# Optimization experiments

Hardware: AMD Instinct MI355X
Metric: run time of the kernel (lower is better)

Reference implementation:

```python
import jax, jax.numpy as jnp
import numpy as np

D_MODEL = 1024
D_K = 1024
B, T = 4, 2048


def setup_inputs() -> dict:
    key = jax.random.key(0)
    kx, kq, kk, kv = jax.random.split(key, 4)
    s = 1.0 / np.sqrt(D_MODEL)
    return {
        "x": jax.random.normal(kx, (B, T, D_MODEL), dtype=jnp.float32),
        "W_q": jax.random.normal(kq, (D_MODEL, D_K), dtype=jnp.float32) * s,
        "W_k": jax.random.normal(kk, (D_MODEL, D_K), dtype=jnp.float32) * s,
        "W_v": jax.random.normal(kv, (D_MODEL, D_K), dtype=jnp.float32) * s,
    }


def reference(x, W_q, W_k, W_v):
    # x: (B, T, C); W_*: (C, d_k). Linear(no bias) == x @ W
    q = jnp.einsum('btc,ck->btk', x, W_q)
    k = jnp.einsum('btc,ck->btk', x, W_k)
    v = jnp.einsum('btc,ck->btk', x, W_v)
    d_k = W_q.shape[1]
    scores = jnp.einsum('bqk,bsk->bqs', q, k) / jnp.sqrt(jnp.asarray(d_k, x.dtype))
    T_ = x.shape[1]
    causal = jnp.tril(jnp.ones((T_, T_), dtype=bool))
    scores = jnp.where(causal, scores, jnp.asarray(-jnp.inf, scores.dtype))
    weights = jax.nn.softmax(scores, axis=-1)
    return jnp.einsum('bqs,bsk->bqk', weights, v)
```

## Files before the change

kernel.cpp:

```cpp
#include <hip/hip_runtime.h>
#include <hip/hip_bf16.h>
#include <stdint.h>

typedef __bf16 bf16x8 __attribute__((ext_vector_type(8)));
typedef float  f32x4  __attribute__((ext_vector_type(4)));
typedef unsigned int u32x4 __attribute__((ext_vector_type(4)));

__device__ __forceinline__ unsigned short f2bf(float x) {
    union { float f; unsigned u; } v; v.f = x;
    unsigned r = v.u + 0x7fffu + ((v.u >> 16) & 1u);
    return (unsigned short)(r >> 16);
}

__device__ __forceinline__ float bf2f(unsigned short b) {
    union { unsigned u; float f; } v; v.u = ((unsigned)b) << 16; return v.f;
}

__device__ __forceinline__ void async16(const void* g, void* l) {
    __builtin_amdgcn_global_load_lds(
        (const __attribute__((address_space(1))) void*)g,
        (__attribute__((address_space(3))) void*)l,
        16, 0, 0);
}

template <typename OutT, bool CAUSAL_SKIP, bool KLIMIT, bool VFOLD>
__global__ __launch_bounds__(256, 3) void gemm_bt(
    const unsigned short* __restrict__ A,
    const unsigned short* __restrict__ Bt,
    OutT* __restrict__ C,
    unsigned short* __restrict__ VtOut,
    int M, int N, int K, int lda, int ldb, int ldc,
    int ldvt, int nsplit,
    long long sA, long long sB, long long sC, long long sVt, float scale)
{
    const int bn = blockIdx.x, bz = blockIdx.z;
    const int bm = KLIMIT ? (gridDim.y - 1 - blockIdx.y) : blockIdx.y;
    if (CAUSAL_SKIP && bn > bm) return;

    A  += (long long)bz * sA;
    Bt += (long long)bz * sB;
    C  += (long long)bz * sC;

    const int m0 = bm * 128, n0 = bn * 128;
    const int Keff = KLIMIT ? min(K, (bm + 1) * 128) : K;

    __shared__ __align__(16) unsigned short LDS[2 * 2 * 128 * 32];

    const int tid  = threadIdx.x;
    const int w    = tid >> 6, l = tid & 63;
    const int wr   = w >> 1,  wc = w & 1;
    const int lrow = l & 15,  quad = l >> 4;

    f32x4 acc[4][4] = {};

    const int rA0  = 32 * w + (l >> 2);
    const int cOff = (((l & 3) ^ ((l >> 3) & 3))) * 8;
    const unsigned short* aG0 = A  + (long long)(m0 + rA0)      * lda + cOff;
    const unsigned short* aG1 = A  + (long long)(m0 + rA0 + 16) * lda + cOff;
    const unsigned short* bG0 = Bt + (long long)(n0 + rA0)      * ldb + cOff;
    const unsigned short* bG1 = Bt + (long long)(n0 + rA0 + 16) * ldb + cOff;
    unsigned short* aL = &LDS[(2 * w) * 512 + l * 8];
    unsigned short* bL = aL + 4096;

    const int sl = (lrow >> 1) & 3;

    async16(aG0, aL);
    async16(aG1, aL + 512);
    async16(bG0, bL);
    async16(bG1, bL + 512);

    for (int k0 = 0; k0 < Keff; k0 += 32) {
        const int cur = ((k0 >> 5) & 1) * 8192;
        __syncthreads();

        if (k0 + 32 < Keff) {
            const int nxt = cur ^ 8192;
            async16(aG0 + k0 + 32, aL + nxt);
            async16(aG1 + k0 + 32, aL + nxt + 512);
            async16(bG0 + k0 + 32, bL + nxt);
            async16(bG1 + k0 + 32, bL + nxt + 512);
        }

        const unsigned short* As = &LDS[cur];
        const unsigned short* Bs = &LDS[cur + 4096];
        bf16x8 af[4], bfr[4];
#pragma unroll
        for (int i = 0; i < 4; i++) {
            af[i]  = *(const bf16x8*)&As[(wr * 64 + i * 16 + lrow) * 32 + (quad ^ sl) * 8];
            bfr[i] = *(const bf16x8*)&Bs[(wc * 64 + i * 16 + lrow) * 32 + (quad ^ sl) * 8];
        }
#pragma unroll
        for (int i = 0; i < 4; i++)
#pragma unroll
            for (int j = 0; j < 4; j++)
                acc[i][j] = __builtin_amdgcn_mfma_f32_16x16x32_bf16(af[i], bfr[j], acc[i][j], 0, 0, 0);
    }

    if constexpr (VFOLD) {
        if (n0 >= nsplit) {
            unsigned short* Vp = VtOut + (long long)bz * sVt;
#pragma unroll
            for (int i = 0; i < 4; i++) {
                const int t = m0 + wr * 64 + i * 16 + quad * 4;
#pragma unroll
                for (int j = 0; j < 4; j++) {
                    const int d = (n0 - nsplit) + wc * 64 + j * 16 + lrow;
                    union { unsigned short u[4]; uint2 p; } o;
#pragma unroll
                    for (int r = 0; r < 4; r++) o.u[r] = f2bf(acc[i][j][r] * scale);
                    *(uint2*)(Vp + (long long)d * ldvt + t) = o.p;
                }
            }
            return;
        }
    }

    __syncthreads();

    char* eb = (char*)LDS + w * 2288;
    const int erow = l >> 2, ep = l & 3;

    if constexpr (sizeof(OutT) == 2) {
#pragma unroll
        for (int i = 0; i < 4; i++) {
#pragma unroll
            for (int j = 0; j < 4; j++)
#pragma unroll
                for (int r = 0; r < 4; r++)
                    *(unsigned short*)(eb + (quad * 4 + r) * 144 + (j * 16 + lrow) * 2) =
                        f2bf(acc[i][j][r] * scale);
            const long long gm = m0 + wr * 64 + i * 16 + erow;
#pragma unroll
            for (int c = 0; c < 2; c++) {
                u32x4 d = *(u32x4*)(eb + erow * 144 + ep * 32 + c * 16);
                *(u32x4*)((unsigned short*)C + gm * ldc + (n0 + wc * 64 + ep * 16 + c * 8)) = d;
            }
        }
    } else {
#pragma unroll
        for (int i = 0; i < 4; i++) {
            const long long gm = m0 + wr * 64 + i * 16 + erow;
#pragma unroll
            for (int jc = 0; jc < 2; jc++) {
#pragma unroll
                for (int jj = 0; jj < 2; jj++)
#pragma unroll
                    for (int r = 0; r < 4; r++)
                        *(float*)(eb + (quad * 4 + r) * 144 + (jj * 16 + lrow) * 4) =
                            acc[i][2 * jc + jj][r] * scale;
#pragma unroll
                for (int c = 0; c < 2; c++) {
                    f32x4 d = *(f32x4*)(eb + erow * 144 + ep * 32 + c * 16);
                    *(f32x4*)((float*)C + gm * ldc + (n0 + wc * 64 + jc * 32 + ep * 8 + c * 4)) = d;
                }
            }
        }
    }
}

__global__ __launch_bounds__(256) void cast_f32_bf16(
    const float4* __restrict__ in, unsigned short* __restrict__ out, int n4)
{
    int i = blockIdx.x * 256 + threadIdx.x;
    if (i >= n4) return;
    float4 v = in[i];
    union { unsigned short u[4]; uint2 p; } o;
    o.u[0] = f2bf(v.x); o.u[1] = f2bf(v.y); o.u[2] = f2bf(v.z); o.u[3] = f2bf(v.w);
    *(uint2*)(out + (long long)i * 4) = o.p;
}

__global__ __launch_bounds__(256) void transpose_cast_w3(
    const float* __restrict__ W0, const float* __restrict__ W1,
    const float* __restrict__ W2, unsigned short* __restrict__ out, int n)
{
    const float* in = (blockIdx.z == 0) ? W0 : (blockIdx.z == 1) ? W1 : W2;
    out += (long long)blockIdx.z * n * n;
    __shared__ float tile[32][33];
    const int tx = threadIdx.x, ty = threadIdx.y;
    const int c0 = blockIdx.x * 32, r0 = blockIdx.y * 32;
#pragma unroll
    for (int i = 0; i < 4; i++)
        tile[ty + i * 8][tx] = in[(long long)(r0 + ty + i * 8) * n + c0 + tx];
    __syncthreads();
#pragma unroll
    for (int i = 0; i < 4; i++)
        out[(long long)(c0 + ty + i * 8) * n + r0 + tx] = f2bf(tile[tx][ty + i * 8]);
}

__global__ __launch_bounds__(256) void causal_softmax_bf16(
    const unsigned short* __restrict__ S, unsigned short* __restrict__ P, int T)
{
    const int row = blockIdx.x;
    const int t   = row & (T - 1);
    const int L   = t + 1;
    const unsigned short* s = S + (long long)row * T;
    unsigned short* p = P + (long long)row * T;
    const int tid  = threadIdx.x;
    const int base = tid * 8;

    uint4 raw = *(const uint4*)(s + base);
    unsigned rr[4] = {raw.x, raw.y, raw.z, raw.w};
    float v[8];
#pragma unroll
    for (int k = 0; k < 4; k++) {
        union { unsigned u; float f; } a, b;
        a.u = (rr[k] & 0xFFFFu) << 16;
        b.u = rr[k] & 0xFFFF0000u;
        v[2 * k] = a.f; v[2 * k + 1] = b.f;
    }
    float mx = -3.0e38f;
#pragma unroll
    for (int k = 0; k < 8; k++) {
        if (base + k >= L) v[k] = -3.0e38f;
        mx = fmaxf(mx, v[k]);
    }
#pragma unroll
    for (int off = 32; off; off >>= 1) mx = fmaxf(mx, __shfl_xor(mx, off));
    __shared__ float red[4], red2[4];
    const int wid = tid >> 6, lid = tid & 63;
    if (lid == 0) red[wid] = mx;
    __syncthreads();
    mx = fmaxf(fmaxf(red[0], red[1]), fmaxf(red[2], red[3]));

    float sum = 0.f;
#pragma unroll
    for (int k = 0; k < 8; k++) { v[k] = __expf(v[k] - mx); sum += v[k]; }
#pragma unroll
    for (int off = 32; off; off >>= 1) sum += __shfl_xor(sum, off);
    if (lid == 0) red2[wid] = sum;
    __syncthreads();
    sum = red2[0] + red2[1] + red2[2] + red2[3];
    const float inv = 1.0f / sum;

    union { unsigned short u[8]; uint4 q; } o;
#pragma unroll
    for (int k = 0; k < 8; k++) o.u[k] = f2bf(v[k] * inv);
    *(uint4*)(p + base) = o.q;
}

extern "C" void kernel_launch(void* const* d_in, const int* in_sizes, int n_in,
                              void* d_out, int out_size, void* d_ws, size_t ws_size,
                              hipStream_t stream)
{
    const int B = 4, T = 2048, C = 1024, D = 1024;
    const float* x  = (const float*)d_in[0];
    const float* Wq = (const float*)d_in[1];
    const float* Wk = (const float*)d_in[2];
    const float* Wv = (const float*)d_in[3];
    float* out = (float*)d_out;
    char* ws = (char*)d_ws;

    const size_t MB = 1ull << 20;
    unsigned short* Xbf   = (unsigned short*)(ws + 0);
    unsigned short* WqkvT = (unsigned short*)(ws + 16 * MB);
    unsigned short* QK    = (unsigned short*)(ws + 22 * MB);
    unsigned short* Vt    = (unsigned short*)(ws + 54 * MB);
    unsigned short* Sbf   = (unsigned short*)(ws + 70 * MB);
    unsigned short* P     = (unsigned short*)(ws + 0);

    const long long sX  = (long long)T * C;
    const long long sQK = (long long)T * 2 * D;
    const long long sVt = (long long)D * T;
    const long long sS  = (long long)T * T;
    const long long sO  = (long long)T * D;

    {
        int n4 = B * T * C / 4;
        cast_f32_bf16<<<dim3((n4 + 255) / 256), dim3(256), 0, stream>>>(
            (const float4*)x, Xbf, n4);
    }
    {
        dim3 g(32, 32, 3), b(32, 8);
        transpose_cast_w3<<<g, b, 0, stream>>>(Wq, Wk, Wv, WqkvT, 1024);
    }
    {
        dim3 g(3072 / 128, 2048 / 128, 4), b(256);
        gemm_bt<unsigned short, false, false, true><<<g, b, 0, stream>>>(
            Xbf, WqkvT, QK, Vt, 2048, 3072, 1024, 1024, 1024, 2048,
             T,  2048, sX, 0, sQK, sVt, 1.0f);
    }
    {
        dim3 g(2048 / 128, 2048 / 128, 4), b(256);
        gemm_bt<unsigned short, true, false, false><<<g, b, 0, stream>>>(
            QK, QK + D, Sbf, nullptr, 2048, 2048, 1024, 2 * D, 2 * D, 2048,
            0, 0, sQK, sQK, sS, 0, 0.03125f);
    }
    {
        causal_softmax_bf16<<<dim3(B * T), dim3(256), 0, stream>>>(Sbf, P, T);
    }
    {
        dim3 g(1024 / 128, 2048 / 128, 4), b(256);
        gemm_bt<float, false, true, false><<<g, b, 0, stream>>>(
            P, Vt, out, nullptr, 2048, 1024, 2048, 2048, 2048, 1024,
            0, 0, sS, sVt, sO, 0, 1.0f);
    }
    (void)in_sizes; (void)n_in; (void)out_size; (void)ws_size;
}
```

Measured before the change: 252.3 us.

## Add 256x256-tile QKV projection GEMM with 8-wave ping-pong LDS pipeline

Replaces the 128x128-tile QKV projection GEMM with a dedicated kernel that uses 256x256 output tiles, 512 threads, a double-buffered 128KB LDS ring with swizzled async global-to-LDS loads, and an interleaved load/MFMA schedule with barriers and priority hints. It also remaps block indices for L2 locality. The goal is to raise arithmetic intensity and overlap memory traffic with MFMA work in the largest GEMM. Separately, the launch bound occupancy hint on the generic gemm_bt is raised from 3 to 4, which may constrain registers. Large LDS use limits occupancy to one block per CU, and the grid is only 384 blocks.

```diff
diff --git a/kernel.cpp b/kernel.cpp
--- a/kernel.cpp
+++ b/kernel.cpp
@@ -23,8 +23,165 @@
         16, 0, 0);
 }
 
+__global__ __launch_bounds__(512, 2) void gemm256_qkv(
+    const unsigned short* __restrict__ A,
+    const unsigned short* __restrict__ Bt,
+    unsigned short* __restrict__ C,
+    unsigned short* __restrict__ VtOut,
+    int K, int lda, int ldb, int ldc, int ldvt, int nsplit,
+    long long sA, long long sC, long long sVt)
+{
+    __shared__ __align__(16) char LDS[131072];
+    const int o = blockIdx.y * gridDim.x + blockIdx.x;
+    const int xc = o & 7, rr_ = o >> 3;
+    const int bn = (xc & 3) * 3 + (rr_ % 3);
+    const int bm = (xc >> 2) * 4 + (rr_ / 3);
+    const int bz = blockIdx.z;
+    const int m0 = bm * 256, n0 = bn * 256;
+    const int nt = K >> 6;
+
+    const unsigned short* Ab = A + (long long)bz * sA + (long long)m0 * lda;
+    const unsigned short* Bb = Bt + (long long)n0 * ldb;
+
+    const int tid = threadIdx.x;
+    const int w = tid >> 6, l = tid & 63;
+    const int wr = w >> 2, wc = w & 3;
+    const int lrow = l & 15, quad = l >> 4;
+
+    const int sr  = tid >> 3;
+    const int ssl = (tid & 7) ^ (sr & 7);
+
+    const int sw = lrow & 7;
+    const unsigned slot0 = (unsigned)((quad ^ sw) * 16);
+    const unsigned slot1 = (unsigned)(((4 + quad) ^ sw) * 16);
+    const unsigned aB = (unsigned)(wr * 16384 + lrow * 128);
+    const unsigned bB = (unsigned)(32768 + (wc >> 1) * 16384 + ((wc & 1) * 64 + lrow) * 128);
+
+    f32x4 acc[8][4] = {};
+
+    auto STAGE = [&](int t, int piece) {
+        if (t >= nt) return;
+        char* dst = LDS + ((t & 1) << 16) + (piece << 14) + tid * 16;
+        const unsigned short* G = (piece < 2) ? Ab : Bb;
+        const int ld = (piece < 2) ? lda : ldb;
+        const unsigned short* g = G + (long long)((piece & 1) * 128 + sr) * ld + (t << 6) + ssl * 8;
+        async16(g, dst);
+        async16(g + (long long)64 * ld, dst + 8192);
+    };
+
+    auto LDA4 = [&](bf16x8 (&a)[4][2], unsigned cb, int mh) {
+        const unsigned base = cb + aB + (unsigned)(mh * 8192);
+#pragma unroll
+        for (int i = 0; i < 4; i++) {
+            a[i][0] = *(const bf16x8*)(LDS + base + i * 2048 + slot0);
+            a[i][1] = *(const bf16x8*)(LDS + base + i * 2048 + slot1);
+        }
+    };
+    auto LDB2 = [&](bf16x8 (&b)[2][2], unsigned cb, int nh) {
+        const unsigned base = cb + bB + (unsigned)(nh * 4096);
+#pragma unroll
+        for (int j = 0; j < 2; j++) {
+            b[j][0] = *(const bf16x8*)(LDS + base + j * 2048 + slot0);
+            b[j][1] = *(const bf16x8*)(LDS + base + j * 2048 + slot1);
+        }
+    };
+    auto MMQ = [&](bf16x8 (&a)[4][2], bf16x8 (&b)[2][2], int mh, int nh) {
+#pragma unroll
+        for (int i = 0; i < 4; i++)
+#pragma unroll
+            for (int j = 0; j < 2; j++)
+#pragma unroll
+                for (int ks = 0; ks < 2; ks++)
+                    acc[mh * 4 + i][nh * 2 + j] = __builtin_amdgcn_mfma_f32_16x16x32_bf16(
+                        a[i][ks], b[j][ks], acc[mh * 4 + i][nh * 2 + j], 0, 0, 0);
+    };
+
+#define MIDBAR() do { __builtin_amdgcn_s_barrier(); \
+                      asm volatile("s_waitcnt lgkmcnt(0)" ::: "memory"); \
+                      __builtin_amdgcn_sched_barrier(0); } while (0)
+#define ENDBAR() do { asm volatile("s_waitcnt lgkmcnt(0)" ::: "memory"); \
+                      __builtin_amdgcn_s_barrier(); } while (0)
+#define VM4()    asm volatile("s_waitcnt vmcnt(4)" ::: "memory")
+#define VM0()    asm volatile("s_waitcnt vmcnt(0)" ::: "memory")
+
+    STAGE(0, 0); STAGE(0, 1); STAGE(0, 2); STAGE(0, 3);
+    STAGE(1, 2); STAGE(1, 3);
+    VM4();
+    ENDBAR();
+
+    for (int t = 0; t < nt; t += 2) {
+        bf16x8 a[4][2], b0[2][2], b1[2][2];
+        LDA4(a, 0, 0); LDB2(b0, 0, 0);
+        STAGE(t + 1, 0);
+        MIDBAR(); __builtin_amdgcn_s_setprio(1); MMQ(a, b0, 0, 0); __builtin_amdgcn_s_setprio(0); ENDBAR();
+        LDB2(b1, 0, 1);
+        STAGE(t + 1, 1);
+        MIDBAR(); __builtin_amdgcn_s_setprio(1); MMQ(a, b1, 0, 1); __builtin_amdgcn_s_setprio(0); ENDBAR();
+        LDA4(a, 0, 1);
+        STAGE(t + 2, 2);
+        MIDBAR(); __builtin_amdgcn_s_setprio(1); MMQ(a, b0, 1, 0); __builtin_amdgcn_s_setprio(0); ENDBAR();
+        STAGE(t + 2, 3);
+        MIDBAR(); __builtin_amdgcn_s_setprio(1); MMQ(a, b1, 1, 1); __builtin_amdgcn_s_setprio(0);
+        if (t + 2 < nt) { VM4(); } else { VM0(); }
+        ENDBAR();
+        LDA4(a, 65536, 0); LDB2(b0, 65536, 0);
+        STAGE(t + 2, 0);
+        MIDBAR(); __builtin_amdgcn_s_setprio(1); MMQ(a, b0, 0, 0); __builtin_amdgcn_s_setprio(0); ENDBAR();
+        LDB2(b1, 65536, 1);
+        STAGE(t + 2, 1);
+        MIDBAR(); __builtin_amdgcn_s_setprio(1); MMQ(a, b1, 0, 1); __builtin_amdgcn_s_setprio(0); ENDBAR();
+        LDA4(a, 65536, 1);
+        STAGE(t + 3, 2);
+        MIDBAR(); __builtin_amdgcn_s_setprio(1); MMQ(a, b0, 1, 0); __builtin_amdgcn_s_setprio(0); ENDBAR();
+        STAGE(t + 3, 3);
+        MIDBAR(); __builtin_amdgcn_s_setprio(1); MMQ(a, b1, 1, 1); __builtin_amdgcn_s_setprio(0);
+        if (t + 3 < nt) { VM4(); } else { VM0(); }
+        ENDBAR();
+    }
+#undef MIDBAR
+#undef ENDBAR
+#undef VM4
+#undef VM0
+
+    if (n0 >= nsplit) {
+        unsigned short* Vp = VtOut + (long long)bz * sVt;
+#pragma unroll
+        for (int i = 0; i < 8; i++) {
+            const int trow = m0 + wr * 128 + i * 16 + quad * 4;
+#pragma unroll
+            for (int j = 0; j < 4; j++) {
+                const int d = (n0 - nsplit) + wc * 64 + j * 16 + lrow;
+                union { unsigned short u[4]; uint2 p; } o2;
+#pragma unroll
+                for (int r = 0; r < 4; r++) o2.u[r] = f2bf(acc[i][j][r]);
+                *(uint2*)(Vp + (long long)d * ldvt + trow) = o2.p;
+            }
+        }
+        return;
+    }
+
+    C += (long long)bz * sC;
+    char* eb = LDS + w * 2288;
+    const int erow = l >> 2, ep = l & 3;
+#pragma unroll
+    for (int i = 0; i < 8; i++) {
+#pragma unroll
+        for (int j = 0; j < 4; j++)
+#pragma unroll
+            for (int r = 0; r < 4; r++)
+                *(unsigned short*)(eb + (quad * 4 + r) * 144 + (j * 16 + lrow) * 2) =
+                    f2bf(acc[i][j][r]);
+        const long long gm = m0 + wr * 128 + i * 16 + erow;
+#pragma unroll
+        for (int c = 0; c < 2; c++) {
+            u32x4 d = *(u32x4*)(eb + erow * 144 + ep * 32 + c * 16);
+            *(u32x4*)(C + gm * ldc + (n0 + wc * 64 + ep * 16 + c * 8)) = d;
+        }
+    }
+}
+
 template <typename OutT, bool CAUSAL_SKIP, bool KLIMIT, bool VFOLD>
-__global__ __launch_bounds__(256, 3) void gemm_bt(
+__global__ __launch_bounds__(256, 4) void gemm_bt(
     const unsigned short* __restrict__ A,
     const unsigned short* __restrict__ Bt,
     OutT* __restrict__ C,
@@ -274,10 +431,10 @@
         transpose_cast_w3<<<g, b, 0, stream>>>(Wq, Wk, Wv, WqkvT, 1024);
     }
     {
-        dim3 g(3072 / 128, 2048 / 128, 4), b(256);
-        gemm_bt<unsigned short, false, false, true><<<g, b, 0, stream>>>(
-            Xbf, WqkvT, QK, Vt, 2048, 3072, 1024, 1024, 1024, 2048,
-             T,  2048, sX, 0, sQK, sVt, 1.0f);
+        dim3 g(3072 / 256, 2048 / 256, 4), b(512);
+        gemm256_qkv<<<g, b, 0, stream>>>(
+            Xbf, WqkvT, QK, Vt, 1024, 1024, 1024, 2048,
+             T,  2048, sX, sQK, sVt);
     }
     {
         dim3 g(2048 / 128, 2048 / 128, 4), b(256);
```

Result: no change. 256.5 us (+1.6%).
